# Optimization experiments

Measured on AMD Instinct MI355X. Metric: run time of the kernel, lower is better.

The kernel has to match this reference:

```python
import jax, jax.numpy as jnp
import numpy as np
import math

D_MODEL = 512
NUM_CLASSES = 8
MEM_SLOTS = 64
STEPS = 4
DECAY = 0.9
TOPK = 8
SCORE_CLIP = 10.0
VOCAB = 32000
MAX_LEN = 2048
B, T = 32, 2048


def _linear_params(key, d_in, d_out):
    kw, kb = jax.random.split(key)
    W = jax.random.normal(kw, (d_in, d_out), jnp.float32) * (1.0 / math.sqrt(d_in))
    b = jnp.zeros((d_out,), jnp.float32)
    return W, b


def setup_inputs() -> dict:
    key = jax.random.key(0)
    ks = jax.random.split(key, 16)
    inp = {}
    inp["input_ids"] = jax.random.randint(ks[0], (B, T), 0, VOCAB)
    inp["attention_mask"] = jnp.ones((B, T), jnp.int32)
    inp["token_emb"] = jax.random.normal(ks[1], (VOCAB, D_MODEL), jnp.float32) * 0.02
    inp["pos_emb"] = jax.random.normal(ks[2], (MAX_LEN, D_MODEL), jnp.float32) * 0.02
    inp["memory_init"] = jax.random.normal(ks[3], (1, MEM_SLOTS, D_MODEL), jnp.float32) * 0.02
    names = ["q", "k", "v", "write", "gate", "rq", "rk", "rv"]
    for i, n in enumerate(names):
        W, b = _linear_params(ks[4 + i], D_MODEL, D_MODEL)
        inp[n + "_W"], inp[n + "_b"] = W, b
    inp["fuse_W"], inp["fuse_b"] = _linear_params(ks[12], 2 * D_MODEL, D_MODEL)
    inp["cls_W"], inp["cls_b"] = _linear_params(ks[13], D_MODEL, NUM_CLASSES)
    inp["tln_g"] = jnp.ones((D_MODEL,), jnp.float32)
    inp["tln_b"] = jnp.zeros((D_MODEL,), jnp.float32)
    inp["mln_g"] = jnp.ones((D_MODEL,), jnp.float32)
    inp["mln_b"] = jnp.zeros((D_MODEL,), jnp.float32)
    return inp


def _layer_norm(x, g, b, eps=1e-5):
    mu = jnp.mean(x, axis=-1, keepdims=True)
    var = jnp.var(x, axis=-1, keepdims=True)
    return (x - mu) * jax.lax.rsqrt(var + eps) * g + b


def _topk_softmax(scores, k):
    # scores: (B, T, S). Equivalent to scatter top-k vals into -inf then softmax:
    # softmax over the top-k entries, zeros elsewhere.
    Bb, Tt, S = scores.shape
    tv, ti = jax.lax.top_k(scores, k)           # (B,T,k)
    w = jax.nn.softmax(tv, axis=-1)
    rows = jnp.arange(Bb * Tt)[:, None]
    out = jnp.zeros((Bb * Tt, S), scores.dtype).at[rows, ti.reshape(-1, k)].set(w.reshape(-1, k))
    return out.reshape(Bb, Tt, S)


def _binding(scores, mask_f, k):
    w = _topk_softmax(jnp.clip(scores, -SCORE_CLIP, SCORE_CLIP), k)
    w = w * mask_f
    return w / jnp.maximum(jnp.sum(w, axis=-1, keepdims=True), 1e-9)


def _forward(input_ids, attention_mask, token_emb, pos_emb, memory_init,
             q_W, q_b, k_W, k_b, v_W, v_b, write_W, write_b, gate_W, gate_b,
             rq_W, rq_b, rk_W, rk_b, rv_W, rv_b, fuse_W, fuse_b,
             cls_W, cls_b, tln_g, tln_b, mln_g, mln_b):
    scale = 1.0 / math.sqrt(D_MODEL)
    tokens = token_emb[input_ids] + pos_emb[jnp.arange(input_ids.shape[1])][None]
    tokens = _layer_norm(tokens, tln_g, tln_b)  # (B,T,D)
    mask_f = attention_mask[..., None].astype(tokens.dtype)  # (B,T,1)
    memory = jnp.broadcast_to(memory_init, (input_ids.shape[0], MEM_SLOTS, D_MODEL))
    for _ in range(STEPS):
        q = tokens @ q_W + q_b
        kk = memory @ k_W + k_b
        scores = jnp.einsum("btd,bsd->bts", q, kk) * scale
        binding = _binding(scores, mask_f, TOPK)  # (B,T,S)
        v = tokens @ v_W + v_b
        write = jnp.einsum("bts,btd->bsd", binding, v)
        slot_usage = jnp.maximum(jnp.sum(binding, axis=1)[..., None], 1e-6)  # (B,S,1)
        write = (write / slot_usage) @ write_W + write_b
        write = jax.nn.sigmoid(write @ gate_W + gate_b) * write
        memory = _layer_norm(DECAY * memory + (1.0 - DECAY) * write, mln_g, mln_b)
    # read
    rq = tokens @ rq_W + rq_b
    rk = memory @ rk_W + rk_b
    rv = memory @ rv_W + rv_b
    scores = jnp.einsum("btd,bsd->bts", rq, rk) * scale
    rw = _binding(scores, mask_f, TOPK)
    context = jnp.einsum("bts,bsd->btd", rw, rv)
    fused = jnp.concatenate([tokens, context], axis=-1) @ fuse_W + fuse_b
    pooled = jnp.sum(fused * mask_f, axis=1) / jnp.maximum(jnp.sum(mask_f, axis=1), 1.0)
    return pooled @ cls_W + cls_b  # (B, C)


def reference(input_ids, attention_mask, token_emb, pos_emb, memory_init,
              q_W, q_b, k_W, k_b, v_W, v_b, write_W, write_b, gate_W, gate_b,
              rq_W, rq_b, rk_W, rk_b, rv_W, rv_b, fuse_W, fuse_b,
              cls_W, cls_b, tln_g, tln_b, mln_g, mln_b):
    return _forward(input_ids, attention_mask, token_emb, pos_emb, memory_init,
                    q_W, q_b, k_W, k_b, v_W, v_b, write_W, write_b, gate_W, gate_b,
                    rq_W, rq_b, rk_W, rk_b, rv_W, rv_b, fuse_W, fuse_b,
                    cls_W, cls_b, tln_g, tln_b, mln_g, mln_b)
```

## Files before the change

### kernel.cpp

```cpp
#include <hip/hip_runtime.h>
#include <hip/hip_bf16.h>
#include <math.h>

#define BB 32
#define TT 2048
#define DM 512
#define SS 64
#define BT (BB*TT)
#define NSTEPS 4
#define SCALE 0.044194173824159216f

typedef unsigned short u16;
typedef unsigned int u32;
typedef __attribute__((ext_vector_type(8))) short s16x8;
typedef __attribute__((ext_vector_type(4))) float f32x4;
typedef __attribute__((ext_vector_type(4))) unsigned u32x4;

__device__ __forceinline__ u16 f2b(float x){
  __hip_bfloat16 h = __float2bfloat16(x);
  return *reinterpret_cast<u16*>(&h);
}
__device__ __forceinline__ float b2f(u16 u){
  __hip_bfloat16 h;
  *reinterpret_cast<u16*>(&h) = u;
  return __bfloat162float(h);
}

static __device__ __forceinline__ float wave_reduce_sum(float v){
  #pragma unroll
  for (int off=32; off; off>>=1) v += __shfl_down(v, off);
  return v;
}

__global__ __launch_bounds__(256) void embed_ln_k(const int* __restrict__ ids,
    const float* __restrict__ temb, const float* __restrict__ pemb,
    const float* __restrict__ g, const float* __restrict__ be, u16* __restrict__ out){
  int w = threadIdx.x>>6, l = threadIdx.x & 63;
  int row0 = blockIdx.x*8 + w*2;
  int row1 = row0 + 1;
  int t0 = row0 & (TT-1), t1 = row1 & (TT-1);
  int id0 = ids[row0], id1 = ids[row1];
  const float* teA = temb + (size_t)id0*DM + l*8;
  const float* peA = pemb + (size_t)t0*DM + l*8;
  const float* teB = temb + (size_t)id1*DM + l*8;
  const float* peB = pemb + (size_t)t1*DM + l*8;
  float4 a0=*(const float4*)teA, a1=*(const float4*)(teA+4);
  float4 c0=*(const float4*)teB, c1=*(const float4*)(teB+4);
  float4 p0=*(const float4*)peA, p1=*(const float4*)(peA+4);
  float4 q0=*(const float4*)peB, q1=*(const float4*)(peB+4);
  float xA[8] = {a0.x+p0.x, a0.y+p0.y, a0.z+p0.z, a0.w+p0.w,
                 a1.x+p1.x, a1.y+p1.y, a1.z+p1.z, a1.w+p1.w};
  float xB[8] = {c0.x+q0.x, c0.y+q0.y, c0.z+q0.z, c0.w+q0.w,
                 c1.x+q1.x, c1.y+q1.y, c1.z+q1.z, c1.w+q1.w};
  float sA1=0.f, sA2=0.f, sB1=0.f, sB2=0.f;
  #pragma unroll
  for (int e=0;e<8;e++){ sA1 += xA[e]; sA2 += xA[e]*xA[e]; sB1 += xB[e]; sB2 += xB[e]*xB[e]; }
  #pragma unroll
  for (int off=1; off<64; off<<=1){
    sA1 += __shfl_xor(sA1, off); sA2 += __shfl_xor(sA2, off);
    sB1 += __shfl_xor(sB1, off); sB2 += __shfl_xor(sB2, off);
  }
  float muA = sA1*(1.f/DM), muB = sB1*(1.f/DM);
  float rsA = rsqrtf(sA2*(1.f/DM) - muA*muA + 1e-5f);
  float rsB = rsqrtf(sB2*(1.f/DM) - muB*muB + 1e-5f);
  const float* gp = g + l*8;
  const float* bp = be + l*8;
  float4 g0=*(const float4*)gp, g1=*(const float4*)(gp+4);
  float4 b0=*(const float4*)bp, b1=*(const float4*)(bp+4);
  float gg[8]={g0.x,g0.y,g0.z,g0.w,g1.x,g1.y,g1.z,g1.w};
  float bb[8]={b0.x,b0.y,b0.z,b0.w,b1.x,b1.y,b1.z,b1.w};
  s16x8 oA, oB;
  #pragma unroll
  for (int e=0;e<8;e++){
    oA[e] = (short)f2b((xA[e]-muA)*rsA*gg[e] + bb[e]);
    oB[e] = (short)f2b((xB[e]-muB)*rsB*gg[e] + bb[e]);
  }
  *(s16x8*)(out + (size_t)row0*DM + l*8) = oA;
  *(s16x8*)(out + (size_t)row1*DM + l*8) = oB;
}

template<int EPI>
__global__ __launch_bounds__(128) void ntgemm_k(const u16* __restrict__ A,
    const u16* __restrict__ Bm, const float* __restrict__ bias,
    const u16* __restrict__ mulb, const float* __restrict__ rowv,
    const float* __restrict__ bias2, void* __restrict__ Cout, float scalep){
  int m0 = blockIdx.x*32 + (threadIdx.x>>6)*16;
  int n0 = blockIdx.y*64;
  int l = threadIdx.x & 63;
  int lr = l & 15, lk = (l>>4)*8;
  const u16* Arow = A + (size_t)(m0 + lr)*512 + lk;
  const u16* B0   = Bm + (size_t)(n0 + lr)*512 + lk;
  f32x4 acc[4] = {};
  #pragma unroll
  for (int k0=0;k0<512;k0+=32){
    s16x8 a = *(const s16x8*)(Arow + k0);
    #pragma unroll
    for (int j=0;j<4;j++){
      s16x8 b = *(const s16x8*)(B0 + (size_t)j*16*512 + k0);
      acc[j] = __builtin_amdgcn_mfma_f32_16x16x32_bf16(a, b, acc[j], 0,0,0);
    }
  }
  int mbase = m0 + (l>>4)*4;
  #pragma unroll
  for (int j=0;j<4;j++){
    int n = n0 + j*16 + lr;
    #pragma unroll
    for (int r=0;r<4;r++){
      int m = mbase + r;
      float v = acc[j][r];
      if (EPI==2){
        float z = v + bias[n];
        float sg = 1.f/(1.f + expf(-z));
        ((float*)Cout)[(size_t)m*512 + n] = b2f(mulb[(size_t)m*512 + n]) * sg;
      }
      if (EPI==3){ ((float*)Cout)[(size_t)m*512 + n] = v + bias[n]; }
      if (EPI==5){ ((u16*)Cout)[(size_t)m*512 + n] = f2b(v + rowv[m]*bias[n] + bias2[n]); }
    }
  }
}

__global__ __launch_bounds__(128) void ptcb_k(const u16* __restrict__ A,
    const u16* __restrict__ Bm, const float* __restrict__ bias,
    const float* __restrict__ mem, const float* __restrict__ wcb,
    const float* __restrict__ cb0p, u16* __restrict__ Pt, float* __restrict__ cb){
  int l = threadIdx.x & 63;
  if (blockIdx.y < 8){
    int m0 = blockIdx.x*32 + (threadIdx.x>>6)*16;
    int n0 = blockIdx.y*64;
    int lr = l & 15, lk = (l>>4)*8;
    const u16* Arow = A + (size_t)(m0 + lr)*512 + lk;
    const u16* B0   = Bm + (size_t)(n0 + lr)*512 + lk;
    f32x4 acc[4] = {};
    #pragma unroll
    for (int k0=0;k0<512;k0+=32){
      s16x8 a = *(const s16x8*)(Arow + k0);
      #pragma unroll
      for (int j=0;j<4;j++){
        s16x8 b = *(const s16x8*)(B0 + (size_t)j*16*512 + k0);
        acc[j] = __builtin_amdgcn_mfma_f32_16x16x32_bf16(a, b, acc[j], 0,0,0);
      }
    }
    int mbase = m0 + (l>>4)*4;
    #pragma unroll
    for (int j=0;j<4;j++){
      int n = n0 + j*16 + lr;
      #pragma unroll
      for (int r=0;r<4;r++)
        Pt[(size_t)(mbase+r)*512 + n] = f2b(acc[j][r] + bias[n]);
    }
  } else {
    int base = blockIdx.x*32 + (threadIdx.x>>6)*16;
    for (int i=0;i<16;i++){
      int row = base + i;
      const float* r = mem + (size_t)row*512;
      float s = 0.f;
      #pragma unroll
      for (int k=0;k<8;k++) s += r[l + 64*k]*wcb[l + 64*k];
      #pragma unroll
      for (int off=32; off; off>>=1) s += __shfl_xor(s, off);
      if (l==0) cb[row] = s + cb0p[0];
    }
  }
}

__global__ __launch_bounds__(64) void bind_k(const u16* __restrict__ tok,
    const u16* __restrict__ Pt, const float* __restrict__ cbuf, const int* __restrict__ mask,
    u16* __restrict__ BNDT, float* __restrict__ cspart){
  int b = blockIdx.y, t0 = blockIdx.x*64;
  int l = threadIdx.x;
  int lr = l&15, g = l>>4, lk = g*8;
  __shared__ float sc[64*66];
  __shared__ u16 bt[64*66];

  const u16* Abase = tok + ((size_t)(b*TT + t0 + lr))*512 + lk;
  const u16* Bbase = Pt + ((size_t)(b*SS + lr))*512 + lk;
  f32x4 acc[4][4] = {};
  #pragma unroll
  for (int k0=0;k0<512;k0+=32){
    s16x8 a[4], bb[4];
    #pragma unroll
    for (int mi=0;mi<4;mi++) a[mi] = *(const s16x8*)(Abase + (size_t)mi*16*512 + k0);
    #pragma unroll
    for (int nj=0;nj<4;nj++) bb[nj] = *(const s16x8*)(Bbase + (size_t)nj*16*512 + k0);
    #pragma unroll
    for (int mi=0;mi<4;mi++)
      #pragma unroll
      for (int nj=0;nj<4;nj++)
        acc[mi][nj] = __builtin_amdgcn_mfma_f32_16x16x32_bf16(a[mi], bb[nj], acc[mi][nj], 0,0,0);
  }
  float cbv[4];
  #pragma unroll
  for (int nj=0;nj<4;nj++) cbv[nj] = cbuf[b*SS + 16*nj + lr];
  #pragma unroll
  for (int mi=0;mi<4;mi++)
    #pragma unroll
    for (int nj=0;nj<4;nj++)
      #pragma unroll
      for (int r=0;r<4;r++){
        float x = acc[mi][nj][r] + cbv[nj];
        x = fminf(fmaxf(x, -10.f), 10.f);
        sc[(16*mi + 4*g + r)*66 + 16*nj + lr] = x;
      }

  float sv[64];
  #pragma unroll
  for (int j=0;j<64;j++) sv[j] = sc[l*66 + j];

  u32 work[64];
  #pragma unroll
  for (int j=0;j<64;j++){
    u32 s = __float_as_uint(sv[j]);
    u32 o = s ^ ((u32)(((int)s) >> 31) | 0x80000000u);
    work[j] = (o & 0xFFFFFFC0u) | (u32)(63 - j);
  }
  u32 mtop = 0;
  #pragma unroll
  for (int it=0; it<8; ++it){
    u32 a[32];
    #pragma unroll
    for (int j=0;j<32;j++){ u32 x = work[2*j], y = work[2*j+1]; a[j] = x>y?x:y; }
    #pragma unroll
    for (int lvl=16; lvl>=1; lvl>>=1)
      #pragma unroll
      for (int j=0;j<lvl;j++){ u32 x = a[2*j], y = a[2*j+1]; a[j] = x>y?x:y; }
    u32 m = a[0];
    if (it==0) mtop = m;
    #pragma unroll
    for (int j=0;j<64;j++) work[j] = (work[j]==m) ? 0u : work[j];
  }
  u32 ot = mtop & 0xFFFFFFC0u;
  u32 tb = (ot & 0x80000000u) ? (ot ^ 0x80000000u) : ~ot;
  float T = __uint_as_float(tb);

  float tot = 0.f;
  #pragma unroll
  for (int j=0;j<64;j++){
    float ej = (work[j]==0u) ? expf(sv[j]-T) : 0.f;
    sv[j] = ej;
    tot += ej;
  }
  int mv = mask[b*TT + t0 + l];
  float inv = mv ? 1.f/tot : 0.f;
  #pragma unroll
  for (int j=0;j<64;j++)
    bt[j*66 + l] = f2b(sv[j]*inv);

  const u32* btw = (const u32*)bt;
  u32 rowbuf[32];
  float csum = 0.f;
  #pragma unroll
  for (int w=0;w<32;w++){
    u32 v = btw[l*33 + w];
    rowbuf[w] = v;
    csum += b2f((u16)(v & 0xFFFFu)) + b2f((u16)(v >> 16));
  }
  cspart[((size_t)b*32 + blockIdx.x)*64 + l] = csum;
  u16* dst = BNDT + ((size_t)(b*SS + l))*TT + t0;
  #pragma unroll
  for (int w8=0;w8<8;w8++){
    u32x4 v;
    v[0]=rowbuf[4*w8]; v[1]=rowbuf[4*w8+1]; v[2]=rowbuf[4*w8+2]; v[3]=rowbuf[4*w8+3];
    *(u32x4*)(dst + 8*w8) = v;
  }
}

__global__ __launch_bounds__(64) void csred_k(const float* __restrict__ cspart,
    float* __restrict__ slot, float* __restrict__ rr, float* __restrict__ raw){
  int b = blockIdx.x, s = threadIdx.x;
  float t = 0.f;
  for (int k=0;k<32;k++) t += cspart[((size_t)b*32 + k)*64 + s];
  raw[b*SS+s] = t;
  float sl = fmaxf(t, 1e-6f);
  slot[b*SS+s] = sl;
  rr[b*SS+s] = t/sl;
}

__global__ __launch_bounds__(256) void wt_k(const u16* __restrict__ BNDT,
    const u16* __restrict__ tok, float* __restrict__ part){
  int dgrp = blockIdx.x, b = blockIdx.y, ks = blockIdx.z;
  int tid = threadIdx.x, w = tid>>6, l = tid&63;
  int lr = l&15, lk = (l>>4)*8;
  __shared__ u16 tk[128][72];
  f32x4 acc[8] = {};
  int trow = tid>>2, dseg = (tid&3)*32;
  const u16* tokbase = tok + ((size_t)b*TT)*512 + dgrp*128;
  const u16* Abase = BNDT + ((size_t)(b*SS + 16*w + lr))*TT;
  for (int chunk=0; chunk<8; ++chunk){
    int tb = ks*512 + chunk*64;
    const u16* src = tokbase + (size_t)(tb + trow)*512 + dseg;
    s16x8 v0 = *(const s16x8*)(src);
    s16x8 v1 = *(const s16x8*)(src+8);
    s16x8 v2 = *(const s16x8*)(src+16);
    s16x8 v3 = *(const s16x8*)(src+24);
    #pragma unroll
    for (int e=0;e<8;e++){
      int d0 = dseg+e, d1 = dseg+8+e, d2 = dseg+16+e, d3 = dseg+24+e;
      tk[d0][(trow + 8*((d0>>5)&3)) & 63] = (u16)v0[e];
      tk[d1][(trow + 8*((d1>>5)&3)) & 63] = (u16)v1[e];
      tk[d2][(trow + 8*((d2>>5)&3)) & 63] = (u16)v2[e];
      tk[d3][(trow + 8*((d3>>5)&3)) & 63] = (u16)v3[e];
    }
    __syncthreads();
    #pragma unroll
    for (int kst=0;kst<2;kst++){
      s16x8 a = *(const s16x8*)(Abase + tb + kst*32 + lk);
      #pragma unroll
      for (int nt=0;nt<8;nt++){
        int dd = nt*16 + lr;
        int cb2 = (kst*32 + lk + 8*((dd>>5)&3)) & 63;
        s16x8 bb = *(const s16x8*)&tk[dd][cb2];
        acc[nt] = __builtin_amdgcn_mfma_f32_16x16x32_bf16(a, bb, acc[nt], 0,0,0);
      }
    }
    __syncthreads();
  }
  float* dst = part + (size_t)ks*2048*512 + ((size_t)(b*SS))*512 + dgrp*128;
  #pragma unroll
  for (int nt=0;nt<8;nt++){
    int d = nt*16 + lr;
    #pragma unroll
    for (int r=0;r<4;r++){
      int s = 16*w + (l>>4)*4 + r;
      dst[(size_t)s*512 + d] = acc[nt][r];
    }
  }
}

__global__ __launch_bounds__(256) void wtred_k(const float* __restrict__ part,
    const float* __restrict__ slot, u16* __restrict__ t1h){
  int i = blockIdx.x*256 + threadIdx.x;
  int row = i>>9;
  float v = part[i] + part[i + 2048*512] + part[i + 2*2048*512] + part[i + 3*2048*512];
  t1h[i] = f2b(v / slot[row]);
}

__global__ __launch_bounds__(256) void allconv_k(
    const float* __restrict__ s0, u16* __restrict__ d0,
    const float* __restrict__ s1, u16* __restrict__ d1,
    const float* __restrict__ s2, u16* __restrict__ d2,
    const float* __restrict__ s3, u16* __restrict__ d3,
    const float* __restrict__ s4, u16* __restrict__ d4){
  int sel = blockIdx.x >> 10;
  int i = (blockIdx.x & 1023)*256 + threadIdx.x;
  const float* s; u16* d;
  if (sel==0){s=s0;d=d0;} else if (sel==1){s=s1;d=d1;} else if (sel==2){s=s2;d=d2;}
  else if (sel==3){s=s3;d=d3;} else {s=s4;d=d4;}
  d[i] = f2b(s[i]);
}

__global__ __launch_bounds__(256) void alltconv_k(
    const float* __restrict__ s0, u16* __restrict__ d0,
    const float* __restrict__ s1, u16* __restrict__ d1,
    const float* __restrict__ s2, u16* __restrict__ d2){
  const float* in; u16* out;
  if (blockIdx.z==0){in=s0;out=d0;} else if (blockIdx.z==1){in=s1;out=d1;} else {in=s2;out=d2;}
  __shared__ float t[32][33];
  int c0 = blockIdx.x*32, r0 = blockIdx.y*32;
  int cx = threadIdx.x&31, ry = threadIdx.x>>5;
  #pragma unroll
  for (int i=0;i<4;i++){ int r = ry + i*8; t[r][cx] = in[(size_t)(r0+r)*512 + c0+cx]; }
  __syncthreads();
  #pragma unroll
  for (int i=0;i<4;i++){ int r = ry + i*8; out[(size_t)(c0+r)*512 + r0+cx] = f2b(t[cx][r]); }
}

__global__ __launch_bounds__(128) void pregemm_k(
    const u16* __restrict__ A0, const u16* __restrict__ B0, u16* __restrict__ C0, float p0,
    const u16* __restrict__ A1, const u16* __restrict__ B1, u16* __restrict__ C1, float p1,
    const u16* __restrict__ A2, const u16* __restrict__ B2, u16* __restrict__ C2, float p2){
  const u16* A; const u16* Bm; u16* C; float sp;
  if (blockIdx.z==0){A=A0;Bm=B0;C=C0;sp=p0;}
  else if (blockIdx.z==1){A=A1;Bm=B1;C=C1;sp=p1;}
  else {A=A2;Bm=B2;C=C2;sp=p2;}
  int m0 = blockIdx.x*32 + (threadIdx.x>>6)*16;
  int n0 = blockIdx.y*64;
  int l = threadIdx.x & 63;
  int lr = l & 15, lk = (l>>4)*8;
  const u16* Arow = A + (size_t)(m0 + lr)*512 + lk;
  const u16* Bp   = Bm + (size_t)(n0 + lr)*512 + lk;
  f32x4 acc[4] = {};
  #pragma unroll
  for (int k0=0;k0<512;k0+=32){
    s16x8 a = *(const s16x8*)(Arow + k0);
    #pragma unroll
    for (int j=0;j<4;j++){
      s16x8 b = *(const s16x8*)(Bp + (size_t)j*16*512 + k0);
      acc[j] = __builtin_amdgcn_mfma_f32_16x16x32_bf16(a, b, acc[j], 0,0,0);
    }
  }
  int mbase = m0 + (l>>4)*4;
  #pragma unroll
  for (int j=0;j<4;j++){
    int n = n0 + j*16 + lr;
    #pragma unroll
    for (int r=0;r<4;r++)
      C[(size_t)(mbase+r)*512 + n] = f2b(acc[j][r] * sp);
  }
}

__global__ __launch_bounds__(256) void smalls_k(
    const float* __restrict__ qW, const float* __restrict__ kB, float* __restrict__ bq,
    const float* __restrict__ rqW, const float* __restrict__ rkB, float* __restrict__ bq_r,
    const float* __restrict__ kW, const float* __restrict__ qB, float* __restrict__ wcb,
    const float* __restrict__ rkW, const float* __restrict__ rqB, float* __restrict__ wcb_r,
    const float* __restrict__ wrW, const float* __restrict__ vB, float* __restrict__ bvw,
    float* __restrict__ cb0s){
  int blk = blockIdx.x;
  if (blk < 512){
    int which = blk >> 7;
    const float* W; const float* v; float* out;
    if (which==0){W=qW; v=kB; out=bq;}
    else if (which==1){W=rqW; v=rkB; out=bq_r;}
    else if (which==2){W=kW; v=qB; out=wcb;}
    else {W=rkW; v=rqB; out=wcb_r;}
    int i = (blk&127)*4 + (threadIdx.x>>6), l = threadIdx.x&63;
    const float* r = W + (size_t)i*512;
    float s = 0.f;
    #pragma unroll
    for (int k=0;k<8;k++) s += r[l + 64*k]*v[l + 64*k];
    #pragma unroll
    for (int off=32; off; off>>=1) s += __shfl_xor(s, off);
    if (l==0) out[i] = s * SCALE;
  } else if (blk < 514){
    int n = (blk-512)*256 + threadIdx.x;
    float s = 0.f;
    for (int o=0;o<512;o++) s += vB[o]*wrW[(size_t)o*512 + n];
    bvw[n] = s;
  } else {
    if (threadIdx.x < 128){
      int w = threadIdx.x>>6, l = threadIdx.x&63;
      const float* a = w ? rkB : kB;
      const float* bvec = w ? rqB : qB;
      float s = 0.f;
      #pragma unroll
      for (int k=0;k<8;k++) s += a[l + 64*k]*bvec[l + 64*k];
      #pragma unroll
      for (int off=32; off; off>>=1) s += __shfl_xor(s, off);
      if (l==0) cb0s[w] = s * SCALE;
    }
  }
}

__global__ __launch_bounds__(256) void meminit_k(const float* __restrict__ src,
    float* __restrict__ mem, u16* __restrict__ memh){
  int i = blockIdx.x*256 + threadIdx.x;
  float v = src[i & (SS*DM-1)];
  mem[i] = v;
  memh[i] = f2b(v);
}

__global__ __launch_bounds__(256) void mem_ln_k(float* __restrict__ mem, const float* __restrict__ w3,
    const float* __restrict__ g, const float* __restrict__ be, u16* __restrict__ memh){
  int row = blockIdx.x;
  int d = threadIdx.x;
  float* mrow = mem + (size_t)row*DM;
  const float* wrow = w3 + (size_t)row*DM;
  float x0 = 0.9f*mrow[d]     + 0.1f*wrow[d];
  float x1 = 0.9f*mrow[d+256] + 0.1f*wrow[d+256];
  float s1 = x0+x1, s2 = x0*x0 + x1*x1;
  s1 = wave_reduce_sum(s1); s2 = wave_reduce_sum(s2);
  __shared__ float r1[4], r2[4];
  int lane = d & 63, w = d>>6;
  if (lane==0){ r1[w]=s1; r2[w]=s2; }
  __syncthreads();
  float S1 = r1[0]+r1[1]+r1[2]+r1[3];
  float S2 = r2[0]+r2[1]+r2[2]+r2[3];
  float mu = S1 * (1.f/DM);
  float var = S2*(1.f/DM) - mu*mu;
  float rs = rsqrtf(var + 1e-5f);
  float y0 = (x0-mu)*rs*g[d] + be[d];
  float y1 = (x1-mu)*rs*g[d+256] + be[d+256];
  mrow[d] = y0; mrow[d+256] = y1;
  memh[(size_t)row*DM + d] = f2b(y0);
  memh[(size_t)row*DM + d+256] = f2b(y1);
}

__global__ __launch_bounds__(256) void tokpart_k(const u16* __restrict__ tok,
    const int* __restrict__ mask, float* __restrict__ tp){
  int b = blockIdx.x, sl = blockIdx.y;
  int w = threadIdx.x>>6, l = threadIdx.x&63;
  float acc[8] = {};
  #pragma unroll 4
  for (int i=0;i<32;i++){
    int t = sl*128 + w + 4*i;
    float m = (float)mask[b*TT + t];
    s16x8 v = *(const s16x8*)(tok + ((size_t)(b*TT + t))*512 + l*8);
    #pragma unroll
    for (int e=0;e<8;e++) acc[e] += m*b2f((u16)v[e]);
  }
  float* dst = tp + ((size_t)(b*64 + sl*4 + w))*512 + l*8;
  #pragma unroll
  for (int e=0;e<8;e++) dst[e] = acc[e];
}

__global__ __launch_bounds__(256) void catden_k(const float* __restrict__ tp,
    const float* __restrict__ rws, const float* __restrict__ rv,
    const int* __restrict__ mask, float* __restrict__ cat, float* __restrict__ denomv){
  int b = blockIdx.x, tid = threadIdx.x;
  float dn = 0.f;
  for (int t=tid; t<TT; t+=256) dn += (float)mask[b*TT+t];
  dn = wave_reduce_sum(dn);
  __shared__ float dred[4];
  if ((tid&63)==0) dred[tid>>6]=dn;
  #pragma unroll
  for (int it=0; it<2; ++it){
    int d = tid + it*256;
    float ts = 0.f;
    for (int k=0;k<64;k++) ts += tp[((size_t)(b*64+k))*512 + d];
    cat[(size_t)b*1024 + d] = ts;
    float c = 0.f;
    for (int s=0;s<SS;s++) c += rws[b*SS+s]*rv[((size_t)b*SS+s)*DM + d];
    cat[(size_t)b*1024 + 512 + d] = c;
  }
  __syncthreads();
  if (tid==0) denomv[b] = dred[0]+dred[1]+dred[2]+dred[3];
}

__global__ __launch_bounds__(256) void fuse_k(const float* __restrict__ cat,
    const float* __restrict__ denomv, const float* __restrict__ fuseW,
    const float* __restrict__ fuseb, float* __restrict__ pooled){
  int b = blockIdx.x, n0 = blockIdx.y*64;
  int l = threadIdx.x&63, kc = threadIdx.x>>6;
  int n = n0 + l;
  float acc = 0.f;
  const float* crow = cat + (size_t)b*1024;
  for (int k=kc*256; k<kc*256+256; ++k)
    acc += crow[k]*fuseW[(size_t)k*512 + n];
  __shared__ float red[4][64];
  red[kc][l] = acc;
  __syncthreads();
  if (kc==0){
    float denom = denomv[b];
    float tot = red[0][l]+red[1][l]+red[2][l]+red[3][l];
    pooled[(size_t)b*512 + n] = (tot + denom*fuseb[n]) / fmaxf(denom, 1.f);
  }
}

__global__ __launch_bounds__(256) void cls_k(const float* __restrict__ pooled,
    const float* __restrict__ clsW, const float* __restrict__ clsb, float* __restrict__ out){
  int b = blockIdx.x;
  int c = threadIdx.x&7, kc = threadIdx.x>>3;
  float acc = 0.f;
  const float* prow = pooled + (size_t)b*512;
  for (int d=kc*16; d<kc*16+16; ++d) acc += prow[d]*clsW[d*8+c];
  __shared__ float red[32][8];
  red[kc][c] = acc;
  __syncthreads();
  if (threadIdx.x < 8){
    float tot = 0.f;
    #pragma unroll
    for (int k=0;k<32;k++) tot += red[k][threadIdx.x];
    out[b*8 + threadIdx.x] = tot + clsb[threadIdx.x];
  }
}

extern "C" void kernel_launch(void* const* d_in, const int* in_sizes, int n_in,
                              void* d_out, int out_size, void* d_ws, size_t ws_size,
                              hipStream_t stream){
  (void)in_sizes; (void)n_in; (void)out_size; (void)ws_size;
  const int*   ids   = (const int*)d_in[0];
  const int*   amask = (const int*)d_in[1];
  const float* temb  = (const float*)d_in[2];
  const float* pemb  = (const float*)d_in[3];
  const float* mem0  = (const float*)d_in[4];
  const float* qW=(const float*)d_in[5],  *qB=(const float*)d_in[6];
  const float* kW=(const float*)d_in[7],  *kB=(const float*)d_in[8];
  const float* vW=(const float*)d_in[9],  *vB=(const float*)d_in[10];
  const float* wrW=(const float*)d_in[11],*wrB=(const float*)d_in[12];
  const float* gtW=(const float*)d_in[13],*gtB=(const float*)d_in[14];
  const float* rqW=(const float*)d_in[15],*rqB=(const float*)d_in[16];
  const float* rkW=(const float*)d_in[17],*rkB=(const float*)d_in[18];
  const float* rvW=(const float*)d_in[19],*rvB=(const float*)d_in[20];
  const float* fW=(const float*)d_in[21], *fB=(const float*)d_in[22];
  const float* cW=(const float*)d_in[23], *cB=(const float*)d_in[24];
  const float* tg=(const float*)d_in[25], *tb=(const float*)d_in[26];
  const float* mg=(const float*)d_in[27], *mb=(const float*)d_in[28];

  char* p = (char*)d_ws;
  size_t off = 0;
  auto alloc = [&](size_t bytes)->char*{ char* r = p + off; off += (bytes + 255) & ~(size_t)255; return r; };
  u16*   tokens = (u16*)  alloc((size_t)BT*DM*2);
  u16*   Pt     = (u16*)  alloc((size_t)BB*SS*DM*2);
  u16*   BNDT   = (u16*)  alloc((size_t)BB*SS*TT*2);
  float* cspart = (float*)alloc((size_t)BB*32*64*4);
  float* wtpart = (float*)alloc((size_t)4*2048*512*4);
  u16*   t1h    = (u16*)  alloc((size_t)2048*512*2);
  u16*   zh     = (u16*)  alloc((size_t)2048*512*2);
  float* mem    = (float*)alloc((size_t)BB*SS*DM*4);
  u16*   memh   = (u16*)  alloc((size_t)BB*SS*DM*2);
  u16*   wrWT   = (u16*)  alloc(512*512*2);
  u16*   gtWT   = (u16*)  alloc(512*512*2);
  u16*   rvWT   = (u16*)  alloc(512*512*2);
  u16*   WqkT   = (u16*)  alloc(512*512*2);
  u16*   WqkT_r = (u16*)  alloc(512*512*2);
  u16*   WvwT   = (u16*)  alloc(512*512*2);
  float* bq     = (float*)alloc(512*4);
  float* bq_r   = (float*)alloc(512*4);
  float* wcb    = (float*)alloc(512*4);
  float* wcb_r  = (float*)alloc(512*4);
  float* bvw    = (float*)alloc(512*4);
  float* cb0s   = (float*)alloc(256);
  float* cbuf   = (float*)alloc(2048*4);
  float* slot   = (float*)alloc(2048*4);
  float* rr     = (float*)alloc(2048*4);
  float* raw    = (float*)alloc(2048*4);
  float* catbuf = (float*)alloc((size_t)BB*1024*4);
  float* denomv = (float*)alloc(BB*4);
  float* pooled = (float*)alloc((size_t)BB*512*4);
  float* rv32   = wtpart;
  float* tspart = wtpart + 1048576;
  float* gh32   = wtpart + 2097152;
  u16*   qWb    = (u16*)((char*)wtpart + 12582912);
  u16*   kWb    = qWb + 512*512;
  u16*   rqWb   = kWb + 512*512;
  u16*   rkWb   = rqWb + 512*512;
  u16*   vWb    = (u16*)((char*)wtpart + 14680064);

  allconv_k<<<5120, 256, 0, stream>>>(qW, qWb, kW, kWb, rqW, rqWb, rkW, rkWb, vW, vWb);
  alltconv_k<<<dim3(16,16,3), 256, 0, stream>>>(wrW, wrWT, gtW, gtWT, rvW, rvWT);
  pregemm_k<<<dim3(16,8,3), 128, 0, stream>>>(qWb, kWb, WqkT, SCALE,
                                              rqWb, rkWb, WqkT_r, SCALE,
                                              wrWT, vWb, WvwT, 1.0f);
  smalls_k<<<515, 256, 0, stream>>>(qW, kB, bq, rqW, rkB, bq_r, kW, qB, wcb,
                                    rkW, rqB, wcb_r, wrW, vB, bvw, cb0s);
  embed_ln_k<<<BT/8, 256, 0, stream>>>(ids, temb, pemb, tg, tb, tokens);
  meminit_k<<<(BB*SS*DM)/256, 256, 0, stream>>>(mem0, mem, memh);

  for (int step=0; step<NSTEPS; ++step){
    ptcb_k<<<dim3(64,9), 128, 0, stream>>>(memh, WqkT, bq, mem, wcb, cb0s, Pt, cbuf);
    bind_k<<<dim3(32,32), 64, 0, stream>>>(tokens, Pt, cbuf, amask, BNDT, cspart);
    csred_k<<<32, 64, 0, stream>>>(cspart, slot, rr, raw);
    wt_k<<<dim3(4,32,4), 256, 0, stream>>>(BNDT, tokens, wtpart);
    wtred_k<<<4096, 256, 0, stream>>>(wtpart, slot, t1h);
    ntgemm_k<5><<<dim3(64,8), 128, 0, stream>>>(t1h, WvwT, bvw, nullptr, rr, wrB, zh, 0.f);
    ntgemm_k<2><<<dim3(64,8), 128, 0, stream>>>(zh, gtWT, gtB, zh, nullptr, nullptr, gh32, 0.f);
    mem_ln_k<<<BB*SS, 256, 0, stream>>>(mem, gh32, mg, mb, memh);
  }

  ptcb_k<<<dim3(64,9), 128, 0, stream>>>(memh, WqkT_r, bq_r, mem, wcb_r, cb0s+1, Pt, cbuf);
  bind_k<<<dim3(32,32), 64, 0, stream>>>(tokens, Pt, cbuf, amask, BNDT, cspart);
  csred_k<<<32, 64, 0, stream>>>(cspart, slot, rr, raw);
  ntgemm_k<3><<<dim3(64,8), 128, 0, stream>>>(memh, rvWT, rvB, nullptr, nullptr, nullptr, rv32, 0.f);
  tokpart_k<<<dim3(32,16), 256, 0, stream>>>(tokens, amask, tspart);
  catden_k<<<32, 256, 0, stream>>>(tspart, raw, rv32, amask, catbuf, denomv);
  fuse_k<<<dim3(32,8), 256, 0, stream>>>(catbuf, denomv, fW, fB, pooled);
  cls_k<<<32, 256, 0, stream>>>(pooled, cW, cB, (float*)d_out);
}
```

Before: 569.7 us.

## Halve bind tile, use iterative-threshold top-k, store wt partials in bf16

bind_k now handles 32 tokens per block instead of 64. This doubles the grid and cuts accumulator and register use. The top-k selection becomes a threshold search that finds the k-th largest key by repeated max-below-current, replacing destructive tree reductions. Only 32 lanes run it while the other 32 sit idle. wt_k writes its split-K partials as bf16 instead of fp32, and wtred_k reads them 8 elements at a time, which halves that traffic but loses precision in the partial sums. Workspace offsets are reshuffled to fit.

Measured after the change: 577.2 us. Within noise of the previous version (+1.3%).

```diff
diff --git a/kernel.cpp b/kernel.cpp
--- a/kernel.cpp
+++ b/kernel.cpp
@@ -166,24 +166,25 @@
 __global__ __launch_bounds__(64) void bind_k(const u16* __restrict__ tok,
     const u16* __restrict__ Pt, const float* __restrict__ cbuf, const int* __restrict__ mask,
     u16* __restrict__ BNDT, float* __restrict__ cspart){
-  int b = blockIdx.y, t0 = blockIdx.x*64;
+  int b = blockIdx.y, t0 = blockIdx.x*32;
   int l = threadIdx.x;
   int lr = l&15, g = l>>4, lk = g*8;
-  __shared__ float sc[64*66];
-  __shared__ u16 bt[64*66];
+  __shared__ float sc[32*66];
+  __shared__ u32 btw[64*17];
+  u16* bt = (u16*)btw;
 
   const u16* Abase = tok + ((size_t)(b*TT + t0 + lr))*512 + lk;
   const u16* Bbase = Pt + ((size_t)(b*SS + lr))*512 + lk;
-  f32x4 acc[4][4] = {};
+  f32x4 acc[2][4] = {};
   #pragma unroll
   for (int k0=0;k0<512;k0+=32){
-    s16x8 a[4], bb[4];
-    #pragma unroll
-    for (int mi=0;mi<4;mi++) a[mi] = *(const s16x8*)(Abase + (size_t)mi*16*512 + k0);
+    s16x8 a[2], bb[4];
+    #pragma unroll
+    for (int mi=0;mi<2;mi++) a[mi] = *(const s16x8*)(Abase + (size_t)mi*16*512 + k0);
     #pragma unroll
     for (int nj=0;nj<4;nj++) bb[nj] = *(const s16x8*)(Bbase + (size_t)nj*16*512 + k0);
     #pragma unroll
-    for (int mi=0;mi<4;mi++)
+    for (int mi=0;mi<2;mi++)
       #pragma unroll
       for (int nj=0;nj<4;nj++)
         acc[mi][nj] = __builtin_amdgcn_mfma_f32_16x16x32_bf16(a[mi], bb[nj], acc[mi][nj], 0,0,0);
@@ -192,7 +193,7 @@
   #pragma unroll
   for (int nj=0;nj<4;nj++) cbv[nj] = cbuf[b*SS + 16*nj + lr];
   #pragma unroll
-  for (int mi=0;mi<4;mi++)
+  for (int mi=0;mi<2;mi++)
     #pragma unroll
     for (int nj=0;nj<4;nj++)
       #pragma unroll
@@ -202,65 +203,61 @@
         sc[(16*mi + 4*g + r)*66 + 16*nj + lr] = x;
       }
 
-  float sv[64];
-  #pragma unroll
-  for (int j=0;j<64;j++) sv[j] = sc[l*66 + j];
-
-  u32 work[64];
-  #pragma unroll
-  for (int j=0;j<64;j++){
-    u32 s = __float_as_uint(sv[j]);
-    u32 o = s ^ ((u32)(((int)s) >> 31) | 0x80000000u);
-    work[j] = (o & 0xFFFFFFC0u) | (u32)(63 - j);
-  }
-  u32 mtop = 0;
-  #pragma unroll
-  for (int it=0; it<8; ++it){
-    u32 a[32];
-    #pragma unroll
-    for (int j=0;j<32;j++){ u32 x = work[2*j], y = work[2*j+1]; a[j] = x>y?x:y; }
-    #pragma unroll
-    for (int lvl=16; lvl>=1; lvl>>=1)
-      #pragma unroll
-      for (int j=0;j<lvl;j++){ u32 x = a[2*j], y = a[2*j+1]; a[j] = x>y?x:y; }
-    u32 m = a[0];
-    if (it==0) mtop = m;
-    #pragma unroll
-    for (int j=0;j<64;j++) work[j] = (work[j]==m) ? 0u : work[j];
-  }
-  u32 ot = mtop & 0xFFFFFFC0u;
-  u32 tb = (ot & 0x80000000u) ? (ot ^ 0x80000000u) : ~ot;
-  float T = __uint_as_float(tb);
-
-  float tot = 0.f;
-  #pragma unroll
-  for (int j=0;j<64;j++){
-    float ej = (work[j]==0u) ? expf(sv[j]-T) : 0.f;
-    sv[j] = ej;
-    tot += ej;
-  }
-  int mv = mask[b*TT + t0 + l];
-  float inv = mv ? 1.f/tot : 0.f;
-  #pragma unroll
-  for (int j=0;j<64;j++)
-    bt[j*66 + l] = f2b(sv[j]*inv);
-
-  const u32* btw = (const u32*)bt;
-  u32 rowbuf[32];
+  if (l < 32){
+    u32 key[64];
+    #pragma unroll
+    for (int j=0;j<64;j++){
+      u32 s = __float_as_uint(sc[l*66 + j]);
+      u32 o = s ^ ((u32)(((int)s) >> 31) | 0x80000000u);
+      key[j] = (o & 0xFFFFFFC0u) | (u32)(63 - j);
+    }
+    u32 cur = 0xFFFFFFFFu, mtop = 0u;
+    #pragma unroll
+    for (int it=0; it<8; ++it){
+      u32 mx = 0u;
+      #pragma unroll
+      for (int j=0;j<64;j++){
+        u32 kj = key[j];
+        u32 cand = (kj < cur) ? kj : 0u;
+        mx = (cand > mx) ? cand : mx;
+      }
+      if (it==0) mtop = mx;
+      cur = mx;
+    }
+    u32 kth = cur;
+    u32 otT = mtop & 0xFFFFFFC0u;
+    float T = __uint_as_float((otT & 0x80000000u) ? (otT ^ 0x80000000u) : ~otT);
+    float e[64];
+    float tot = 0.f;
+    #pragma unroll
+    for (int j=0;j<64;j++){
+      u32 ot = key[j] & 0xFFFFFFC0u;
+      float sj = __uint_as_float((ot & 0x80000000u) ? (ot ^ 0x80000000u) : ~ot);
+      float ej = (key[j] >= kth) ? __expf(sj - T) : 0.f;
+      e[j] = ej;
+      tot += ej;
+    }
+    int mv = mask[b*TT + t0 + l];
+    float inv = mv ? 1.f/tot : 0.f;
+    #pragma unroll
+    for (int j=0;j<64;j++)
+      bt[j*34 + l] = f2b(e[j]*inv);
+  }
+  u32 rowbuf[16];
   float csum = 0.f;
   #pragma unroll
-  for (int w=0;w<32;w++){
-    u32 v = btw[l*33 + w];
+  for (int w=0;w<16;w++){
+    u32 v = btw[l*17 + w];
     rowbuf[w] = v;
     csum += b2f((u16)(v & 0xFFFFu)) + b2f((u16)(v >> 16));
   }
-  cspart[((size_t)b*32 + blockIdx.x)*64 + l] = csum;
+  cspart[((size_t)b*64 + blockIdx.x)*64 + l] = csum;
   u16* dst = BNDT + ((size_t)(b*SS + l))*TT + t0;
   #pragma unroll
-  for (int w8=0;w8<8;w8++){
+  for (int w4=0;w4<4;w4++){
     u32x4 v;
-    v[0]=rowbuf[4*w8]; v[1]=rowbuf[4*w8+1]; v[2]=rowbuf[4*w8+2]; v[3]=rowbuf[4*w8+3];
-    *(u32x4*)(dst + 8*w8) = v;
+    v[0]=rowbuf[4*w4]; v[1]=rowbuf[4*w4+1]; v[2]=rowbuf[4*w4+2]; v[3]=rowbuf[4*w4+3];
+    *(u32x4*)(dst + 8*w4) = v;
   }
 }
 
@@ -268,7 +265,7 @@
     float* __restrict__ slot, float* __restrict__ rr, float* __restrict__ raw){
   int b = blockIdx.x, s = threadIdx.x;
   float t = 0.f;
-  for (int k=0;k<32;k++) t += cspart[((size_t)b*32 + k)*64 + s];
+  for (int k=0;k<64;k++) t += cspart[((size_t)b*64 + k)*64 + s];
   raw[b*SS+s] = t;
   float sl = fmaxf(t, 1e-6f);
   slot[b*SS+s] = sl;
@@ -276,7 +273,7 @@
 }
 
 __global__ __launch_bounds__(256) void wt_k(const u16* __restrict__ BNDT,
-    const u16* __restrict__ tok, float* __restrict__ part){
+    const u16* __restrict__ tok, u16* __restrict__ part){
   int dgrp = blockIdx.x, b = blockIdx.y, ks = blockIdx.z;
   int tid = threadIdx.x, w = tid>>6, l = tid&63;
   int lr = l&15, lk = (l>>4)*8;
@@ -314,24 +311,34 @@
     }
     __syncthreads();
   }
-  float* dst = part + (size_t)ks*2048*512 + ((size_t)(b*SS))*512 + dgrp*128;
+  u16* dst = part + (size_t)ks*2048*512 + ((size_t)(b*SS))*512 + dgrp*128;
   #pragma unroll
   for (int nt=0;nt<8;nt++){
     int d = nt*16 + lr;
     #pragma unroll
     for (int r=0;r<4;r++){
       int s = 16*w + (l>>4)*4 + r;
-      dst[(size_t)s*512 + d] = acc[nt][r];
-    }
-  }
-}
-
-__global__ __launch_bounds__(256) void wtred_k(const float* __restrict__ part,
+      dst[(size_t)s*512 + d] = f2b(acc[nt][r]);
+    }
+  }
+}
+
+__global__ __launch_bounds__(256) void wtred_k(const u16* __restrict__ part,
     const float* __restrict__ slot, u16* __restrict__ t1h){
-  int i = blockIdx.x*256 + threadIdx.x;
+  int i = (blockIdx.x*256 + threadIdx.x)*8;
   int row = i>>9;
-  float v = part[i] + part[i + 2048*512] + part[i + 2*2048*512] + part[i + 3*2048*512];
-  t1h[i] = f2b(v / slot[row]);
+  float inv = 1.f / slot[row];
+  s16x8 p0 = *(const s16x8*)(part + i);
+  s16x8 p1 = *(const s16x8*)(part + i + 2048*512);
+  s16x8 p2 = *(const s16x8*)(part + i + 2*2048*512);
+  s16x8 p3 = *(const s16x8*)(part + i + 3*2048*512);
+  s16x8 o;
+  #pragma unroll
+  for (int e=0;e<8;e++){
+    float v = b2f((u16)p0[e]) + b2f((u16)p1[e]) + b2f((u16)p2[e]) + b2f((u16)p3[e]);
+    o[e] = (short)f2b(v * inv);
+  }
+  *(s16x8*)(t1h + i) = o;
 }
 
 __global__ __launch_bounds__(256) void allconv_k(
@@ -582,7 +589,7 @@
   u16*   tokens = (u16*)  alloc((size_t)BT*DM*2);
   u16*   Pt     = (u16*)  alloc((size_t)BB*SS*DM*2);
   u16*   BNDT   = (u16*)  alloc((size_t)BB*SS*TT*2);
-  float* cspart = (float*)alloc((size_t)BB*32*64*4);
+  float* cspart = (float*)alloc((size_t)BB*64*64*4);
   float* wtpart = (float*)alloc((size_t)4*2048*512*4);
   u16*   t1h    = (u16*)  alloc((size_t)2048*512*2);
   u16*   zh     = (u16*)  alloc((size_t)2048*512*2);
@@ -607,14 +614,16 @@
   float* catbuf = (float*)alloc((size_t)BB*1024*4);
   float* denomv = (float*)alloc(BB*4);
   float* pooled = (float*)alloc((size_t)BB*512*4);
-  float* rv32   = wtpart;
-  float* tspart = wtpart + 1048576;
-  float* gh32   = wtpart + 2097152;
+  u16*   wtp16  = (u16*)wtpart;
+  float* rv32   = wtpart + 2621440;
+  float* tspart = wtpart + 2621440 + 1048576;
+  float* gh32   = (float*)((char*)wtpart + 2097152*4 + 0);
   u16*   qWb    = (u16*)((char*)wtpart + 12582912);
   u16*   kWb    = qWb + 512*512;
   u16*   rqWb   = kWb + 512*512;
   u16*   rkWb   = rqWb + 512*512;
   u16*   vWb    = (u16*)((char*)wtpart + 14680064);
+  gh32 = (float*)((char*)wtpart + 8912896);
 
   allconv_k<<<5120, 256, 0, stream>>>(qW, qWb, kW, kWb, rqW, rqWb, rkW, rkWb, vW, vWb);
   alltconv_k<<<dim3(16,16,3), 256, 0, stream>>>(wrW, wrWT, gtW, gtWT, rvW, rvWT);
@@ -628,17 +637,17 @@
 
   for (int step=0; step<NSTEPS; ++step){
     ptcb_k<<<dim3(64,9), 128, 0, stream>>>(memh, WqkT, bq, mem, wcb, cb0s, Pt, cbuf);
-    bind_k<<<dim3(32,32), 64, 0, stream>>>(tokens, Pt, cbuf, amask, BNDT, cspart);
+    bind_k<<<dim3(64,32), 64, 0, stream>>>(tokens, Pt, cbuf, amask, BNDT, cspart);
     csred_k<<<32, 64, 0, stream>>>(cspart, slot, rr, raw);
-    wt_k<<<dim3(4,32,4), 256, 0, stream>>>(BNDT, tokens, wtpart);
-    wtred_k<<<4096, 256, 0, stream>>>(wtpart, slot, t1h);
+    wt_k<<<dim3(4,32,4), 256, 0, stream>>>(BNDT, tokens, wtp16);
+    wtred_k<<<512, 256, 0, stream>>>(wtp16, slot, t1h);
     ntgemm_k<5><<<dim3(64,8), 128, 0, stream>>>(t1h, WvwT, bvw, nullptr, rr, wrB, zh, 0.f);
     ntgemm_k<2><<<dim3(64,8), 128, 0, stream>>>(zh, gtWT, gtB, zh, nullptr, nullptr, gh32, 0.f);
     mem_ln_k<<<BB*SS, 256, 0, stream>>>(mem, gh32, mg, mb, memh);
   }
 
   ptcb_k<<<dim3(64,9), 128, 0, stream>>>(memh, WqkT_r, bq_r, mem, wcb_r, cb0s+1, Pt, cbuf);
-  bind_k<<<dim3(32,32), 64, 0, stream>>>(tokens, Pt, cbuf, amask, BNDT, cspart);
+  bind_k<<<dim3(64,32), 64, 0, stream>>>(tokens, Pt, cbuf, amask, BNDT, cspart);
   csred_k<<<32, 64, 0, stream>>>(cspart, slot, rr, raw);
   ntgemm_k<3><<<dim3(64,8), 128, 0, stream>>>(memh, rvWT, rvB, nullptr, nullptr, nullptr, rv32, 0.f);
   tokpart_k<<<dim3(32,16), 256, 0, stream>>>(tokens, amask, tspart);
```
